# Optimization experiments

Hardware: AMD Instinct MI355X
Metric: run time of the kernel (lower is better)

## Reference

```python
import jax, jax.numpy as jnp
import numpy as np

B, T, N, F = 4, 24, 4096, 128
DIM, DIM_ATTN, RANK, HEAD = 128, 128, 32, 4
HEAD_DIM = DIM_ATTN // HEAD


def setup_inputs() -> dict:
    key = jax.random.key(0)
    ks = jax.random.split(key, 6)
    x = jax.random.normal(ks[0], (B, T, N, F), dtype=jnp.float32)
    # nn.Linear(dim, dim_attn): weight (out, in), bias (out,)
    Wq = jax.random.normal(ks[1], (DIM_ATTN, DIM), dtype=jnp.float32) / np.sqrt(DIM)
    bq = jnp.zeros((DIM_ATTN,), dtype=jnp.float32)
    # low-rank key parameter (rank, head, head_dim)
    key_param = jax.random.normal(ks[2], (RANK, HEAD, HEAD_DIM), dtype=jnp.float32)
    # nn.Linear(dim, dim)
    Wv = jax.random.normal(ks[3], (DIM, DIM), dtype=jnp.float32) / np.sqrt(DIM)
    bv = jnp.zeros((DIM,), dtype=jnp.float32)
    alpha = jnp.full((HEAD, 1), np.log(9.0), dtype=jnp.float32)
    beta = jnp.full((HEAD, 1), np.log(0.01), dtype=jnp.float32)
    return {"x": x, "Wq": Wq, "bq": bq, "key_param": key_param,
            "Wv": Wv, "bv": bv, "alpha": alpha, "beta": beta}


def reference(x, Wq, bq, key_param, Wv, bv, alpha, beta):
    b, t, n, f = x.shape
    q = (x @ Wq.T + bq).reshape(b, t, n, HEAD, HEAD_DIM)
    # scores over the rank dimension
    attn = jnp.einsum('btnhd,rhd->btnhr', q, key_param) / np.sqrt(HEAD_DIM)
    xv = (x @ Wv.T + bv).reshape(b, t, n, HEAD, HEAD_DIM)
    # stage 1: softmax over rank (last axis), aggregate values into rank slots
    v = jnp.einsum('btnhr,btnhd->btrhd', jax.nn.softmax(attn, axis=-1), xv)
    # stage 2: softmax over nodes (axis -3 == n), redistribute to nodes
    v = jnp.einsum('btnhr,btrhd->btnhd', jax.nn.softmax(attn, axis=-3), v)
    # sigmoid-gated residual mix; alpha/beta (head,1) broadcast over d
    v = jax.nn.sigmoid(alpha) * xv + jax.nn.sigmoid(beta) * v
    return v.reshape(b, t, n, f)
```

## Files before the change

kernel.cpp:

```cpp
#include <hip/hip_runtime.h>

constexpr int Nn = 4096, Fc = 128;
constexpr int Rr = 32, Hh = 4, Dd = 32;
constexpr int BT = 96;
constexpr float SCALE = 0.17677669529663687f;

constexpr size_t OFF_V1  = 0;
constexpr size_t OFF_Z   = (size_t)BT * Hh * Rr * Dd;
constexpr size_t OFF_BQK = OFF_Z + (size_t)BT * Hh * Rr;
constexpr size_t OFF_V1Z = OFF_BQK + 128;
constexpr size_t OFF_U   = OFF_V1Z + (size_t)BT * Hh * Dd * Rr / 2;

constexpr int U_WKHI = 0, U_WVHI = 16384, U_WVLO = 32768;

using short8  = __attribute__((ext_vector_type(8))) short;
using floatx4 = __attribute__((ext_vector_type(4))) float;

__device__ inline ushort f2bf(float f) {
    union { float f; unsigned u; } c{f};
    unsigned r = c.u + 0x7fffu + ((c.u >> 16) & 1u);
    return (ushort)(r >> 16);
}
__device__ inline float bf2f(ushort u) {
    union { unsigned u; float f; } c{(unsigned)u << 16};
    return c.f;
}

__global__ void kprep(const float* __restrict__ Wq, const float* __restrict__ bq,
                      const float* __restrict__ Wv, const float* __restrict__ key,
                      ushort* __restrict__ U, float* __restrict__ bqk)
{
    const int idx = blockIdx.x * 256 + threadIdx.x;
    if (idx < 16384) {
        const int hr = idx >> 7, f = idx & 127;
        const int h = hr >> 5, r = hr & 31;
        float s = 0.f;
#pragma unroll
        for (int d = 0; d < 32; d++)
            s += Wq[(h * 32 + d) * 128 + f] * key[(r * 4 + h) * 32 + d];
        U[U_WKHI + idx] = f2bf(s);
    } else if (idx < 32768) {
        const int o = idx - 16384;
        const float v = Wv[o];
        const ushort h = f2bf(v);
        U[U_WVHI + o] = h;
        U[U_WVLO + o] = f2bf(v - bf2f(h));
    } else if (idx < 32768 + 128) {
        const int hr = idx - 32768;
        const int h = hr >> 5, r = hr & 31;
        float s = 0.f;
#pragma unroll
        for (int d = 0; d < 32; d++)
            s += bq[h * 32 + d] * key[(r * 4 + h) * 32 + d];
        bqk[hr] = s;
    }
}

__global__ __launch_bounds__(256, 2)
void ka(const float* __restrict__ x, const float* __restrict__ bv,
        const ushort* __restrict__ U, const float* __restrict__ bqk,
        float* __restrict__ v1, float* __restrict__ Z)
{
    __shared__ __align__(16) char lds[71680];

    const int t = threadIdx.x;
    const int w = t >> 6, lane = t & 63;
    const int quad = lane >> 4, l15 = lane & 15;
    const int bt = blockIdx.y;
    constexpr int NT = 4;

    char* wsc = lds + 34816 + w * 9216;
    ushort* eT  = (ushort*)wsc;
    ushort* xvT = (ushort*)(wsc + 4608);

    const ushort* WKh = U + U_WKHI;
    const ushort* Wvh = U + U_WVHI;

    float bvv[2], bqkv[2];
#pragma unroll
    for (int i = 0; i < 2; i++) {
        bvv[i]  = bv[32 * w + 16 * i + l15];
        bqkv[i] = bqk[32 * w + 16 * i + l15];
    }

    floatx4 accV1[2][2];
#pragma unroll
    for (int i = 0; i < 2; i++)
#pragma unroll
        for (int j = 0; j < 2; j++) accV1[i][j] = (floatx4)0.f;
    float zacc[2] = {0.f, 0.f};

    const float* xbase = x + ((size_t)bt * Nn + blockIdx.x * (NT * 64)) * Fc;

    float4 xr[8];
#pragma unroll
    for (int i = 0; i < 8; i++) xr[i] = ((const float4*)xbase)[i * 256 + t];

#pragma unroll 1
    for (int it = 0; it < NT; ++it) {
        ushort* xh = (ushort*)(lds + (it & 1) * 17408);
#pragma unroll
        for (int i = 0; i < 8; i++) {
            const int idx = i * 256 + t;
            const int row = idx >> 5, c4 = idx & 31;
            float4 v = xr[i];
            ushort4 hv;
            hv.x = f2bf(v.x); hv.y = f2bf(v.y); hv.z = f2bf(v.z); hv.w = f2bf(v.w);
            *(ushort4*)&xh[row * 136 + c4 * 4] = hv;
        }
        __syncthreads();

        floatx4 acca[4][2], accv[4][2];
#pragma unroll
        for (int mt = 0; mt < 4; mt++)
#pragma unroll
            for (int nt = 0; nt < 2; nt++) {
                acca[mt][nt] = (floatx4)0.f;
                accv[mt][nt] = (floatx4)0.f;
            }

#pragma unroll
        for (int kc = 0; kc < 4; kc++) {
            short8 ah[4];
#pragma unroll
            for (int mt = 0; mt < 4; mt++)
                ah[mt] = *(const short8*)&xh[(16 * mt + l15) * 136 + kc * 32 + quad * 8];
            short8 kb2[2], vb[2];
#pragma unroll
            for (int nt = 0; nt < 2; nt++) {
                const int off = (32 * w + 16 * nt + l15) * 128 + kc * 32 + quad * 8;
                kb2[nt] = *(const short8*)&WKh[off];
                vb[nt]  = *(const short8*)&Wvh[off];
            }
#pragma unroll
            for (int mt = 0; mt < 4; mt++)
#pragma unroll
                for (int nt = 0; nt < 2; nt++) {
                    acca[mt][nt] = __builtin_amdgcn_mfma_f32_16x16x32_bf16(ah[mt], kb2[nt], acca[mt][nt], 0, 0, 0);
                    accv[mt][nt] = __builtin_amdgcn_mfma_f32_16x16x32_bf16(ah[mt], vb[nt],  accv[mt][nt], 0, 0, 0);
                }
        }

        if (it + 1 < NT) {
            const float4* xg = (const float4*)(xbase + (size_t)(it + 1) * 64 * Fc);
#pragma unroll
            for (int i = 0; i < 8; i++) xr[i] = xg[i * 256 + t];
        }

        float sloc[4][4];
#pragma unroll
        for (int mt = 0; mt < 4; mt++)
#pragma unroll
            for (int reg = 0; reg < 4; reg++) {
                const int n = 16 * mt + 4 * quad + reg;
                const float e0 = __expf((acca[mt][0][reg] + bqkv[0]) * SCALE);
                const float e1 = __expf((acca[mt][1][reg] + bqkv[1]) * SCALE);
                eT[l15 * 72 + n]        = f2bf(e0);
                eT[(16 + l15) * 72 + n] = f2bf(e1);
                zacc[0] += e0; zacc[1] += e1;
                sloc[mt][reg] = e0 + e1;
            }
#pragma unroll
        for (int m = 1; m < 16; m <<= 1)
#pragma unroll
            for (int mt = 0; mt < 4; mt++)
#pragma unroll
                for (int reg = 0; reg < 4; reg++)
                    sloc[mt][reg] += __shfl_xor(sloc[mt][reg], m);

#pragma unroll
        for (int mt = 0; mt < 4; mt++)
#pragma unroll
            for (int reg = 0; reg < 4; reg++) {
                const int n = 16 * mt + 4 * quad + reg;
                const float sw = 1.f / sloc[mt][reg];
#pragma unroll
                for (int nt = 0; nt < 2; nt++)
                    xvT[(16 * nt + l15) * 72 + n] =
                        f2bf((accv[mt][nt][reg] + bvv[nt]) * sw);
            }

#pragma unroll
        for (int kn = 0; kn < 2; kn++) {
            short8 ae[2], bx[2];
#pragma unroll
            for (int i = 0; i < 2; i++) {
                ae[i] = *(const short8*)&eT[(16 * i + l15) * 72 + kn * 32 + quad * 8];
                bx[i] = *(const short8*)&xvT[(16 * i + l15) * 72 + kn * 32 + quad * 8];
            }
#pragma unroll
            for (int mt = 0; mt < 2; mt++)
#pragma unroll
                for (int nt = 0; nt < 2; nt++)
                    accV1[mt][nt] = __builtin_amdgcn_mfma_f32_16x16x32_bf16(ae[mt], bx[nt], accV1[mt][nt], 0, 0, 0);
        }
    }

#pragma unroll
    for (int rt = 0; rt < 2; rt++) {
        float zr = zacc[rt];
        zr += __shfl_xor(zr, 16);
        zr += __shfl_xor(zr, 32);
        if (quad == 0)
            atomicAdd(&Z[((size_t)bt * Hh + w) * Rr + 16 * rt + l15], zr);
    }
    float* v1b = v1 + ((size_t)bt * Hh + w) * Rr * Dd;
#pragma unroll
    for (int mt = 0; mt < 2; mt++)
#pragma unroll
        for (int nt = 0; nt < 2; nt++)
#pragma unroll
            for (int reg = 0; reg < 4; reg++)
                atomicAdd(&v1b[(16 * mt + 4 * quad + reg) * 32 + 16 * nt + l15],
                          accV1[mt][nt][reg]);
}

__global__ void k2b(const float* __restrict__ v1, const float* __restrict__ Z,
                    ushort* __restrict__ v1z)
{
    const int idx = blockIdx.x * 256 + threadIdx.x;
    const int d = idx & 31, r = (idx >> 5) & 31, hr = idx >> 10;
    const float z = Z[hr * 32 + r];
    v1z[((size_t)hr * 32 + d) * 32 + r] = f2bf(v1[idx] / z);
}

__global__ __launch_bounds__(256, 2)
void kb(const float* __restrict__ x, const float* __restrict__ bv,
        const ushort* __restrict__ U, const float* __restrict__ bqk,
        const ushort* __restrict__ v1z, const float* __restrict__ alpha,
        const float* __restrict__ beta, float* __restrict__ out)
{
    __shared__ __align__(16) char lds[67584];
    ushort* xhi = (ushort*)lds;
    ushort* xlo = (ushort*)(lds + 17408);

    const int t = threadIdx.x;
    const int w = t >> 6, lane = t & 63;
    const int quad = lane >> 4, l15 = lane & 15;
    const int bt = blockIdx.y;
    constexpr int NT = 4;

    char* wsc = lds + 34816 + w * 8192;
    ushort* eS = (ushort*)wsc;
    float*  fS = (float*)wsc;

    const ushort* WKh = U + U_WKHI;
    const ushort* Wvh = U + U_WVHI;
    const ushort* Wvl = U + U_WVLO;

    float bqkv[2], bvv[2];
#pragma unroll
    for (int i = 0; i < 2; i++) {
        bqkv[i] = bqk[32 * w + 16 * i + l15];
        bvv[i]  = bv[32 * w + 16 * i + l15];
    }
    short8 vbz[2];
#pragma unroll
    for (int dt = 0; dt < 2; dt++)
        vbz[dt] = *(const short8*)&v1z[(((size_t)bt * Hh + w) * Dd + 16 * dt + l15) * Rr + quad * 8];
    const float sa = 1.f / (1.f + __expf(-alpha[w]));
    const float sb = 1.f / (1.f + __expf(-beta[w]));

    const float* xbase = x + ((size_t)bt * Nn + blockIdx.x * (NT * 64)) * Fc;
    float* obase = out + ((size_t)bt * Nn + blockIdx.x * (NT * 64)) * Fc;

    float4 xr[8];
#pragma unroll
    for (int i = 0; i < 8; i++) xr[i] = ((const float4*)xbase)[i * 256 + t];

#pragma unroll 1
    for (int it = 0; it < NT; ++it) {
#pragma unroll
        for (int i = 0; i < 8; i++) {
            const int idx = i * 256 + t;
            const int row = idx >> 5, c4 = idx & 31;
            float4 v = xr[i];
            ushort h0 = f2bf(v.x), h1 = f2bf(v.y), h2 = f2bf(v.z), h3 = f2bf(v.w);
            ushort4 hv; hv.x = h0; hv.y = h1; hv.z = h2; hv.w = h3;
            ushort4 lv; lv.x = f2bf(v.x - bf2f(h0)); lv.y = f2bf(v.y - bf2f(h1));
            lv.z = f2bf(v.z - bf2f(h2)); lv.w = f2bf(v.w - bf2f(h3));
            *(ushort4*)&xhi[row * 136 + c4 * 4] = hv;
            *(ushort4*)&xlo[row * 136 + c4 * 4] = lv;
        }
        __syncthreads();

        floatx4 acca[4][2], accv[4][2];
#pragma unroll
        for (int mt = 0; mt < 4; mt++)
#pragma unroll
            for (int nt = 0; nt < 2; nt++) {
                acca[mt][nt] = (floatx4)0.f;
                accv[mt][nt] = (floatx4)0.f;
            }

#pragma unroll
        for (int kc = 0; kc < 4; kc++) {
            short8 ahi[4], alo[4];
#pragma unroll
            for (int mt = 0; mt < 4; mt++) {
                const int ro = (16 * mt + l15) * 136 + kc * 32 + quad * 8;
                ahi[mt] = *(const short8*)&xhi[ro];
                alo[mt] = *(const short8*)&xlo[ro];
            }
            short8 kb2[2], vbh[2], vbl[2];
#pragma unroll
            for (int nt = 0; nt < 2; nt++) {
                const int off = (32 * w + 16 * nt + l15) * 128 + kc * 32 + quad * 8;
                kb2[nt] = *(const short8*)&WKh[off];
                vbh[nt] = *(const short8*)&Wvh[off];
                vbl[nt] = *(const short8*)&Wvl[off];
            }
#pragma unroll
            for (int mt = 0; mt < 4; mt++)
#pragma unroll
                for (int nt = 0; nt < 2; nt++) {
                    acca[mt][nt] = __builtin_amdgcn_mfma_f32_16x16x32_bf16(ahi[mt], kb2[nt], acca[mt][nt], 0, 0, 0);
                    accv[mt][nt] = __builtin_amdgcn_mfma_f32_16x16x32_bf16(ahi[mt], vbh[nt], accv[mt][nt], 0, 0, 0);
                    accv[mt][nt] = __builtin_amdgcn_mfma_f32_16x16x32_bf16(ahi[mt], vbl[nt], accv[mt][nt], 0, 0, 0);
                    accv[mt][nt] = __builtin_amdgcn_mfma_f32_16x16x32_bf16(alo[mt], vbh[nt], accv[mt][nt], 0, 0, 0);
                }
        }

        if (it + 1 < NT) {
            const float4* xg = (const float4*)(xbase + (size_t)(it + 1) * 64 * Fc);
#pragma unroll
            for (int i = 0; i < 8; i++) xr[i] = xg[i * 256 + t];
        }

#pragma unroll
        for (int mt = 0; mt < 4; mt++)
#pragma unroll
            for (int rt = 0; rt < 2; rt++)
#pragma unroll
                for (int reg = 0; reg < 4; reg++) {
                    const int row = 16 * mt + 4 * quad + reg;
                    const int col = 16 * rt + l15;
                    eS[row * 40 + col] =
                        f2bf(__expf((acca[mt][rt][reg] + bqkv[rt]) * SCALE));
                }

        short8 pa[4];
#pragma unroll
        for (int mt = 0; mt < 4; mt++)
            pa[mt] = *(const short8*)&eS[(16 * mt + l15) * 40 + quad * 8];
        floatx4 acc2[4][2];
#pragma unroll
        for (int mt = 0; mt < 4; mt++)
#pragma unroll
            for (int dt = 0; dt < 2; dt++) {
                acc2[mt][dt] = (floatx4)0.f;
                acc2[mt][dt] = __builtin_amdgcn_mfma_f32_16x16x32_bf16(pa[mt], vbz[dt], acc2[mt][dt], 0, 0, 0);
            }

#pragma unroll
        for (int mt = 0; mt < 4; mt++)
#pragma unroll
            for (int nt = 0; nt < 2; nt++)
#pragma unroll
                for (int reg = 0; reg < 4; reg++) {
                    const int row = 16 * mt + 4 * quad + reg;
                    const int col = 16 * nt + l15;
                    fS[row * 32 + col] =
                        sa * (accv[mt][nt][reg] + bvv[nt]) + sb * acc2[mt][nt][reg];
                }
        float* op = obase + (size_t)it * 64 * Fc;
#pragma unroll
        for (int i = 0; i < 8; i++) {
            const int idx = i * 64 + lane;
            const int n = idx >> 3, c4 = idx & 7;
            *(float4*)&op[(size_t)n * 128 + w * 32 + c4 * 4] =
                *(const float4*)&fS[n * 32 + c4 * 4];
        }
        __syncthreads();
    }
}

extern "C" void kernel_launch(void* const* d_in, const int* in_sizes, int n_in,
                              void* d_out, int out_size, void* d_ws, size_t ws_size,
                              hipStream_t stream)
{
    const float* x     = (const float*)d_in[0];
    const float* Wq    = (const float*)d_in[1];
    const float* bq    = (const float*)d_in[2];
    const float* key   = (const float*)d_in[3];
    const float* Wv    = (const float*)d_in[4];
    const float* bv    = (const float*)d_in[5];
    const float* alpha = (const float*)d_in[6];
    const float* beta  = (const float*)d_in[7];
    float* out = (float*)d_out;

    float*  ws   = (float*)d_ws;
    float*  v1   = ws + OFF_V1;
    float*  Z    = ws + OFF_Z;
    float*  bqkp = ws + OFF_BQK;
    ushort* v1z  = (ushort*)(ws + OFF_V1Z);
    ushort* U    = (ushort*)(ws + OFF_U);

    hipMemsetAsync(v1, 0,
                   (size_t)(BT * Hh * Rr * Dd + BT * Hh * Rr) * sizeof(float),
                   stream);
    kprep<<<dim3(129), 256, 0, stream>>>(Wq, bq, Wv, key, U, bqkp);
    ka<<<dim3(16, BT), 256, 0, stream>>>(x, bv, U, bqkp, v1, Z);
    k2b<<<dim3(BT * Hh * Rr * Dd / 256), 256, 0, stream>>>(v1, Z, v1z);
    kb<<<dim3(16, BT), 256, 0, stream>>>(x, bv, U, bqkp, v1z, alpha, beta, out);
}
```

Before: 522.6 us.

## Shrink LDS for three-block occupancy and fold v1 normalization into output kernel

Kernel ka drops its double-buffered x tile to a single buffer with an extra barrier and tightens padding, so its LDS footprint fits three blocks per CU under a raised launch bound. The separate k2b normalization kernel is removed, and kb now reads v1 and Z directly, dividing and packing to bf16 in registers. Kb also splits the exp/MFMA stage into halves to shrink its scratch buffer and writes output straight from registers instead of staging through LDS. The trade is an added barrier, the loss of x double buffering, and less-coalesced direct global stores, in exchange for higher occupancy and one fewer launch.

```diff
diff --git a/kernel.cpp b/kernel.cpp
--- a/kernel.cpp
+++ b/kernel.cpp
@@ -8,8 +8,7 @@
 constexpr size_t OFF_V1  = 0;
 constexpr size_t OFF_Z   = (size_t)BT * Hh * Rr * Dd;
 constexpr size_t OFF_BQK = OFF_Z + (size_t)BT * Hh * Rr;
-constexpr size_t OFF_V1Z = OFF_BQK + 128;
-constexpr size_t OFF_U   = OFF_V1Z + (size_t)BT * Hh * Dd * Rr / 2;
+constexpr size_t OFF_U   = OFF_BQK + 128;
 
 constexpr int U_WKHI = 0, U_WVHI = 16384, U_WVLO = 32768;
 
@@ -56,12 +55,13 @@
     }
 }
 
-__global__ __launch_bounds__(256, 2)
+__global__ __launch_bounds__(256, 3)
 void ka(const float* __restrict__ x, const float* __restrict__ bv,
         const ushort* __restrict__ U, const float* __restrict__ bqk,
         float* __restrict__ v1, float* __restrict__ Z)
 {
-    __shared__ __align__(16) char lds[71680];
+    __shared__ __align__(16) char lds[54272];
+    ushort* xh = (ushort*)lds;
 
     const int t = threadIdx.x;
     const int w = t >> 6, lane = t & 63;
@@ -69,9 +69,9 @@
     const int bt = blockIdx.y;
     constexpr int NT = 4;
 
-    char* wsc = lds + 34816 + w * 9216;
+    char* wsc = lds + 17408 + w * 8960;
     ushort* eT  = (ushort*)wsc;
-    ushort* xvT = (ushort*)(wsc + 4608);
+    ushort* xvT = (ushort*)(wsc + 4352);
 
     const ushort* WKh = U + U_WKHI;
     const ushort* Wvh = U + U_WVHI;
@@ -98,7 +98,6 @@
 
 #pragma unroll 1
     for (int it = 0; it < NT; ++it) {
-        ushort* xh = (ushort*)(lds + (it & 1) * 17408);
 #pragma unroll
         for (int i = 0; i < 8; i++) {
             const int idx = i * 256 + t;
@@ -140,6 +139,7 @@
                     accv[mt][nt] = __builtin_amdgcn_mfma_f32_16x16x32_bf16(ah[mt], vb[nt],  accv[mt][nt], 0, 0, 0);
                 }
         }
+        __syncthreads();
 
         if (it + 1 < NT) {
             const float4* xg = (const float4*)(xbase + (size_t)(it + 1) * 64 * Fc);
@@ -155,8 +155,8 @@
                 const int n = 16 * mt + 4 * quad + reg;
                 const float e0 = __expf((acca[mt][0][reg] + bqkv[0]) * SCALE);
                 const float e1 = __expf((acca[mt][1][reg] + bqkv[1]) * SCALE);
-                eT[l15 * 72 + n]        = f2bf(e0);
-                eT[(16 + l15) * 72 + n] = f2bf(e1);
+                eT[l15 * 68 + n]        = f2bf(e0);
+                eT[(16 + l15) * 68 + n] = f2bf(e1);
                 zacc[0] += e0; zacc[1] += e1;
                 sloc[mt][reg] = e0 + e1;
             }
@@ -185,7 +185,7 @@
             short8 ae[2], bx[2];
 #pragma unroll
             for (int i = 0; i < 2; i++) {
-                ae[i] = *(const short8*)&eT[(16 * i + l15) * 72 + kn * 32 + quad * 8];
+                ae[i] = *(const short8*)&eT[(16 * i + l15) * 68 + kn * 32 + quad * 8];
                 bx[i] = *(const short8*)&xvT[(16 * i + l15) * 72 + kn * 32 + quad * 8];
             }
 #pragma unroll
@@ -215,22 +215,14 @@
                           accV1[mt][nt][reg]);
 }
 
-__global__ void k2b(const float* __restrict__ v1, const float* __restrict__ Z,
-                    ushort* __restrict__ v1z)
-{
-    const int idx = blockIdx.x * 256 + threadIdx.x;
-    const int d = idx & 31, r = (idx >> 5) & 31, hr = idx >> 10;
-    const float z = Z[hr * 32 + r];
-    v1z[((size_t)hr * 32 + d) * 32 + r] = f2bf(v1[idx] / z);
-}
-
-__global__ __launch_bounds__(256, 2)
+__global__ __launch_bounds__(256, 3)
 void kb(const float* __restrict__ x, const float* __restrict__ bv,
         const ushort* __restrict__ U, const float* __restrict__ bqk,
-        const ushort* __restrict__ v1z, const float* __restrict__ alpha,
-        const float* __restrict__ beta, float* __restrict__ out)
+        const float* __restrict__ v1, const float* __restrict__ Z,
+        const float* __restrict__ alpha, const float* __restrict__ beta,
+        float* __restrict__ out)
 {
-    __shared__ __align__(16) char lds[67584];
+    __shared__ __align__(16) char lds[45056];
     ushort* xhi = (ushort*)lds;
     ushort* xlo = (ushort*)(lds + 17408);
 
@@ -240,9 +232,7 @@
     const int bt = blockIdx.y;
     constexpr int NT = 4;
 
-    char* wsc = lds + 34816 + w * 8192;
-    ushort* eS = (ushort*)wsc;
-    float*  fS = (float*)wsc;
+    ushort* eS = (ushort*)(lds + 34816 + w * 2560);
 
     const ushort* WKh = U + U_WKHI;
     const ushort* Wvh = U + U_WVHI;
@@ -254,10 +244,24 @@
         bqkv[i] = bqk[32 * w + 16 * i + l15];
         bvv[i]  = bv[32 * w + 16 * i + l15];
     }
+
+    const float* v1h = v1 + ((size_t)bt * Hh + w) * Rr * Dd;
+    const float* Zh  = Z + ((size_t)bt * Hh + w) * Rr;
+    float zr8[8];
+#pragma unroll
+    for (int j = 0; j < 8; j++) zr8[j] = 1.f / Zh[8 * quad + j];
     short8 vbz[2];
 #pragma unroll
-    for (int dt = 0; dt < 2; dt++)
-        vbz[dt] = *(const short8*)&v1z[(((size_t)bt * Hh + w) * Dd + 16 * dt + l15) * Rr + quad * 8];
+    for (int dt = 0; dt < 2; dt++) {
+        union { short8 s; unsigned u[4]; } uu;
+#pragma unroll
+        for (int jj = 0; jj < 4; jj++) {
+            const float a0 = v1h[(8 * quad + 2 * jj) * 32 + 16 * dt + l15] * zr8[2 * jj];
+            const float a1 = v1h[(8 * quad + 2 * jj + 1) * 32 + 16 * dt + l15] * zr8[2 * jj + 1];
+            uu.u[jj] = ((unsigned)f2bf(a1) << 16) | f2bf(a0);
+        }
+        vbz[dt] = uu.s;
+    }
     const float sa = 1.f / (1.f + __expf(-alpha[w]));
     const float sb = 1.f / (1.f + __expf(-beta[w]));
 
@@ -320,6 +324,7 @@
                     accv[mt][nt] = __builtin_amdgcn_mfma_f32_16x16x32_bf16(alo[mt], vbh[nt], accv[mt][nt], 0, 0, 0);
                 }
         }
+        __syncthreads();
 
         if (it + 1 < NT) {
             const float4* xg = (const float4*)(xbase + (size_t)(it + 1) * 64 * Fc);
@@ -327,51 +332,44 @@
             for (int i = 0; i < 8; i++) xr[i] = xg[i * 256 + t];
         }
 
+        floatx4 acc2[4][2];
+#pragma unroll
+        for (int half = 0; half < 2; half++) {
+#pragma unroll
+            for (int mtl = 0; mtl < 2; mtl++) {
+                const int mt = 2 * half + mtl;
+#pragma unroll
+                for (int rt = 0; rt < 2; rt++)
+#pragma unroll
+                    for (int reg = 0; reg < 4; reg++) {
+                        const int row = 16 * mtl + 4 * quad + reg;
+                        eS[row * 40 + 16 * rt + l15] =
+                            f2bf(__expf((acca[mt][rt][reg] + bqkv[rt]) * SCALE));
+                    }
+            }
+#pragma unroll
+            for (int mtl = 0; mtl < 2; mtl++) {
+                const int mt = 2 * half + mtl;
+                short8 pa = *(const short8*)&eS[(16 * mtl + l15) * 40 + quad * 8];
+#pragma unroll
+                for (int dt = 0; dt < 2; dt++) {
+                    acc2[mt][dt] = (floatx4)0.f;
+                    acc2[mt][dt] = __builtin_amdgcn_mfma_f32_16x16x32_bf16(pa, vbz[dt], acc2[mt][dt], 0, 0, 0);
+                }
+            }
+        }
+
+        float* op = obase + (size_t)it * 64 * Fc;
 #pragma unroll
         for (int mt = 0; mt < 4; mt++)
 #pragma unroll
-            for (int rt = 0; rt < 2; rt++)
+            for (int nt = 0; nt < 2; nt++)
 #pragma unroll
                 for (int reg = 0; reg < 4; reg++) {
                     const int row = 16 * mt + 4 * quad + reg;
-                    const int col = 16 * rt + l15;
-                    eS[row * 40 + col] =
-                        f2bf(__expf((acca[mt][rt][reg] + bqkv[rt]) * SCALE));
-                }
-
-        short8 pa[4];
-#pragma unroll
-        for (int mt = 0; mt < 4; mt++)
-            pa[mt] = *(const short8*)&eS[(16 * mt + l15) * 40 + quad * 8];
-        floatx4 acc2[4][2];
-#pragma unroll
-        for (int mt = 0; mt < 4; mt++)
-#pragma unroll
-            for (int dt = 0; dt < 2; dt++) {
-                acc2[mt][dt] = (floatx4)0.f;
-                acc2[mt][dt] = __builtin_amdgcn_mfma_f32_16x16x32_bf16(pa[mt], vbz[dt], acc2[mt][dt], 0, 0, 0);
-            }
-
-#pragma unroll
-        for (int mt = 0; mt < 4; mt++)
-#pragma unroll
-            for (int nt = 0; nt < 2; nt++)
-#pragma unroll
-                for (int reg = 0; reg < 4; reg++) {
-                    const int row = 16 * mt + 4 * quad + reg;
-                    const int col = 16 * nt + l15;
-                    fS[row * 32 + col] =
+                    op[(size_t)row * 128 + w * 32 + 16 * nt + l15] =
                         sa * (accv[mt][nt][reg] + bvv[nt]) + sb * acc2[mt][nt][reg];
                 }
-        float* op = obase + (size_t)it * 64 * Fc;
-#pragma unroll
-        for (int i = 0; i < 8; i++) {
-            const int idx = i * 64 + lane;
-            const int n = idx >> 3, c4 = idx & 7;
-            *(float4*)&op[(size_t)n * 128 + w * 32 + c4 * 4] =
-                *(const float4*)&fS[n * 32 + c4 * 4];
-        }
-        __syncthreads();
     }
 }
 
@@ -391,16 +389,14 @@
 
     float*  ws   = (float*)d_ws;
     float*  v1   = ws + OFF_V1;
-    float*  Z    = ws + OFF_Z;
+    float*  Zb   = ws + OFF_Z;
     float*  bqkp = ws + OFF_BQK;
-    ushort* v1z  = (ushort*)(ws + OFF_V1Z);
     ushort* U    = (ushort*)(ws + OFF_U);
 
     hipMemsetAsync(v1, 0,
                    (size_t)(BT * Hh * Rr * Dd + BT * Hh * Rr) * sizeof(float),
                    stream);
     kprep<<<dim3(129), 256, 0, stream>>>(Wq, bq, Wv, key, U, bqkp);
-    ka<<<dim3(16, BT), 256, 0, stream>>>(x, bv, U, bqkp, v1, Z);
-    k2b<<<dim3(BT * Hh * Rr * Dd / 256), 256, 0, stream>>>(v1, Z, v1z);
-    kb<<<dim3(16, BT), 256, 0, stream>>>(x, bv, U, bqkp, v1z, alpha, beta, out);
-}
+    ka<<<dim3(16, BT), 256, 0, stream>>>(x, bv, U, bqkp, v1, Zb);
+    kb<<<dim3(16, BT), 256, 0, stream>>>(x, bv, U, bqkp, v1, Zb, alpha, beta, out);
+}
```

After: 696.9 us. +33.4%, slower.
